# Optimization experiments

Hardware: AMD Instinct MI355X
Metric: run time of the kernel (lower is better)

The kernel has to match this reference:

```python
import jax, jax.numpy as jnp
import numpy as np

# Static configuration (matches init_kwargs)
L = 3264          # seq_length
K = 12            # ktc=4 -> K=12
LOCC = 4          # ktc=4 -> Locc=4
S, B, A = 8, 64, 4  # streams (user/port pairs), batch, rx antennas
DELAY_MIN, DELAY_MAX = -10, 10


def _phasor(m):
    # m: integer shifts [S, B] -> exp(1j*2*pi*m*n/L) as [S, B, L]
    n = jnp.arange(L, dtype=jnp.int32)
    ang = (2.0 * np.pi / L) * ((m[..., None] * n) % L).astype(jnp.float32)
    return jax.lax.complex(jnp.cos(ang), jnp.sin(ang))


def _linear_interp(h_avg):
    # np.interp with uniform source grid orig[i] = (LOCC-1)/2 + i*LOCC, clamped at ends.
    # h_avg: [S, B, A, R] complex, R = L // LOCC -> [S, B, A, L]
    R = L // LOCC
    new = jnp.arange(L, dtype=jnp.float32)
    t = jnp.clip((new - (LOCC - 1) / 2.0) / LOCC, 0.0, float(R - 1))
    i0 = jnp.floor(t).astype(jnp.int32)
    i1 = jnp.minimum(i0 + 1, R - 1)
    frac = (t - i0).astype(jnp.float32)
    return h_avg[..., i0] * (1.0 - frac) + h_avg[..., i1] * frac


def reference(ls_real, ls_imag, cyclic_shifts, noise_powers):
    ls = jax.lax.complex(ls_real, ls_imag)                     # [S,B,A,L]
    ideal_peak = ((K - cyclic_shifts) % K) * (L // K)          # [S]

    # Stage 1: IFFT + timing-offset search (torch.no_grad in original)
    h_time = jnp.fft.ifft(ls, axis=-1)
    power = jax.lax.stop_gradient(jnp.sum(jnp.abs(h_time) ** 2, axis=2))  # [S,B,L]
    offs = jnp.arange(DELAY_MIN, DELAY_MAX + 1, dtype=jnp.int32)          # [21]
    cand_idx = (ideal_peak[:, None] + offs[None, :]) % L                   # [S,21]
    cand_idx = jnp.broadcast_to(cand_idx[:, None, :], (S, B, offs.shape[0]))
    cand_pow = jnp.take_along_axis(power, cand_idx, axis=-1)               # [S,B,21]
    t_off = offs[jnp.argmax(cand_pow, axis=-1)]                            # [S,B]
    m = t_off + ideal_peak[:, None]                                        # [S,B]
    ph_m = _phasor(m)        # [S,B,L]
    ph_T = _phasor(t_off)    # [S,B,L]

    # Stage 2: phasor shift, OCC demux, interpolation (inside no_grad in original)
    h_shift = ls * ph_m[:, :, None, :]
    h_avg = h_shift.reshape(S, B, A, L // LOCC, LOCC).mean(-1)             # [S,B,A,L/4]
    h_interp = jax.lax.stop_gradient(_linear_interp(h_avg))                # [S,B,A,L]

    # Stage 3: global residual against stream (0,0)'s LS estimate
    total_recon = jnp.sum(h_interp * jnp.conj(ph_m)[:, :, None, :], axis=0)  # [B,A,L]
    residual = ls[0] - total_recon                                           # [B,A,L]

    # Stage 4: apply residual, MMSE (identity: mmse_module=None), timing recovery
    h_wr = h_interp + residual[None, :, :, None, :].squeeze(3) if False else h_interp + residual[None] * ph_m[:, :, None, :]
    final = h_wr * jnp.conj(ph_T)[:, :, None, :]                             # [S,B,A,L]
    return jnp.stack([final.real, final.imag]).astype(jnp.float32)          # [2,S,B,A,L]


def setup_inputs() -> dict:
    key = jax.random.key(0)
    k1, k2, k3, k4 = jax.random.split(key, 4)
    return {
        "ls_real": jax.random.normal(k1, (S, B, A, L), dtype=jnp.float32),
        "ls_imag": jax.random.normal(k2, (S, B, A, L), dtype=jnp.float32),
        "cyclic_shifts": jax.random.randint(k3, (S,), 0, K, dtype=jnp.int32),
        "noise_powers": jax.random.uniform(k4, (B,), dtype=jnp.float32),
    }
```

## Files before the change

kernel.cpp:

```cpp
#include <hip/hip_runtime.h>

namespace {

constexpr int L = 3264;
constexpr int K = 12;
constexpr int S = 8;
constexpr int B = 64;
constexpr int A = 4;
constexpr int R = 816;
constexpr int NOFF = 21;
constexpr int PEAK_STEP = L / K;
constexpr float TWO_PI = 6.28318530717958647692f;
constexpr float CINV = TWO_PI / (float)L;
constexpr int NCHUNK = (L + 255) / 256;

__device__ __forceinline__ float rfl(float x) {
    return __uint_as_float(__builtin_amdgcn_readfirstlane(__float_as_uint(x)));
}

__global__ __launch_bounds__(256)
void k_table(float2* __restrict__ tw)
{
    const int j = blockIdx.x * 256 + threadIdx.x;
    if (j < L) {
        float sv, cv;
        __sincosf(CINV * (float)j, &sv, &cv);
        tw[j] = make_float2(cv, sv);
    }
}

__global__ __launch_bounds__(256)
void k_dft(const float* __restrict__ lsr, const float* __restrict__ lsi,
           const int* __restrict__ cs, float* __restrict__ pow_out)
{
    __shared__ float2 red[4][NOFF];

    const int blk = blockIdx.x;
    const int sb = blk >> 2;
    const int a = blk & 3;
    const int s = sb >> 6;
    const int tid = threadIdx.x;
    const int lane = tid & 63;
    const int w = tid >> 6;

    const int ideal = ((K - cs[s]) % K) * PEAK_STEP;
    int idx0 = (ideal - 10) % L; if (idx0 < 0) idx0 += L;

    const int jb = (tid * idx0) % L;
    float br, bi; __sincosf(CINV * (float)jb, &bi, &br);
    float lr, li; __sincosf(CINV * (float)tid, &li, &lr);
    float pwr[NOFF], pwi[NOFF], ar[NOFF], ai[NOFF];
    pwr[0] = br; pwi[0] = bi;
    #pragma unroll
    for (int d = 1; d < NOFF; ++d) {
        pwr[d] = pwr[d-1] * lr - pwi[d-1] * li;
        pwi[d] = pwr[d-1] * li + pwi[d-1] * lr;
    }
    #pragma unroll
    for (int d = 0; d < NOFF; ++d) { ar[d] = 0.f; ai[d] = 0.f; }

    const int js = (256 * idx0) % L;
    float s0r, s0i; __sincosf(CINV * (float)js, &s0i, &s0r);
    float c8r, c8i; __sincosf(CINV * 256.0f, &c8i, &c8r);
    float str_[NOFF], sti_[NOFF];
    {
        float cr = s0r, ci = s0i;
        #pragma unroll
        for (int d = 0; d < NOFF; ++d) {
            str_[d] = rfl(cr); sti_[d] = rfl(ci);
            const float nr2 = cr * c8r - ci * c8i;
            ci = cr * c8i + ci * c8r;
            cr = nr2;
        }
    }

    const float* __restrict__ pr  = lsr + (size_t)blk * L;
    const float* __restrict__ pi_ = lsi + (size_t)blk * L;

    for (int it = 0; it < 12; ++it) {
        const float xr = pr[tid + (it << 8)];
        const float xi = pi_[tid + (it << 8)];
        #pragma unroll
        for (int d = 0; d < NOFF; ++d) {
            ar[d] += xr * pwr[d] - xi * pwi[d];
            ai[d] += xr * pwi[d] + xi * pwr[d];
            const float nr2 = pwr[d] * str_[d] - pwi[d] * sti_[d];
            pwi[d] = pwr[d] * sti_[d] + pwi[d] * str_[d];
            pwr[d] = nr2;
        }
    }
    if (tid < 192) {
        const float xr = pr[tid + 3072];
        const float xi = pi_[tid + 3072];
        #pragma unroll
        for (int d = 0; d < NOFF; ++d) {
            ar[d] += xr * pwr[d] - xi * pwi[d];
            ai[d] += xr * pwi[d] + xi * pwr[d];
        }
    }

    #pragma unroll
    for (int d = 0; d < NOFF; ++d) {
        float r = ar[d], im = ai[d];
        #pragma unroll
        for (int o = 32; o > 0; o >>= 1) {
            r  += __shfl_xor(r, o);
            im += __shfl_xor(im, o);
        }
        if (lane == 0) red[w][d] = make_float2(r, im);
    }
    __syncthreads();

    if (w == 0 && lane < NOFF) {
        float rr = 0.f, ii = 0.f;
        #pragma unroll
        for (int q = 0; q < 4; ++q) { rr += red[q][lane].x; ii += red[q][lane].y; }
        pow_out[sb * (NOFF * A) + lane * A + a] = rr * rr + ii * ii;
    }
}

__global__ __launch_bounds__(64)
void k_argmax(const float* __restrict__ pow_in, const int* __restrict__ cs,
              int* __restrict__ toff_out, int* __restrict__ m_out)
{
    const int sb = blockIdx.x;
    const int lane = threadIdx.x;
    const int s = sb >> 6;
    const int ideal = ((K - cs[s]) % K) * PEAK_STEP;

    float pw = -1.f;
    if (lane < NOFF) {
        const float4 p4 = *(const float4*)(pow_in + sb * (NOFF * A) + lane * A);
        pw = p4.x + p4.y + p4.z + p4.w;
    }
    float mx = pw;
    #pragma unroll
    for (int o = 32; o > 0; o >>= 1) mx = fmaxf(mx, __shfl_xor(mx, o));
    const unsigned long long msk = __ballot(pw == mx);
    const int argd = __ffsll(msk) - 1;
    if (lane == 0) {
        const int toff = argd - 10;
        toff_out[sb] = toff;
        m_out[sb]    = toff + ideal;
    }
}

__global__ __launch_bounds__(256)
void k_havg(const float* __restrict__ lsr, const float* __restrict__ lsi,
            const int* __restrict__ m_arr, const float2* __restrict__ tw,
            float2* __restrict__ havg)
{
    const int blk = blockIdx.x;
    const int sb = blk >> 2;
    const int tid = threadIdx.x;

    int mp = m_arr[sb] % L; if (mp < 0) mp += L;
    const float2 emp = tw[mp];

    const float4* __restrict__ qr4 = (const float4*)(lsr + (size_t)blk * L);
    const float4* __restrict__ qi4 = (const float4*)(lsi + (size_t)blk * L);
    float2* __restrict__ dst = havg + (size_t)blk * R;

    for (int i = tid; i < R; i += 256) {
        const int j = (mp * (4 * i)) % L;
        const float2 w0 = tw[j];
        const float4 xr = qr4[i];
        const float4 xi = qi4[i];
        float wr = w0.x, wi = w0.y;
        float are, aim, nr;
        are  = xr.x * wr - xi.x * wi;  aim  = xr.x * wi + xi.x * wr;
        nr = wr * emp.x - wi * emp.y;  wi = wr * emp.y + wi * emp.x;  wr = nr;
        are += xr.y * wr - xi.y * wi;  aim += xr.y * wi + xi.y * wr;
        nr = wr * emp.x - wi * emp.y;  wi = wr * emp.y + wi * emp.x;  wr = nr;
        are += xr.z * wr - xi.z * wi;  aim += xr.z * wi + xi.z * wr;
        nr = wr * emp.x - wi * emp.y;  wi = wr * emp.y + wi * emp.x;  wr = nr;
        are += xr.w * wr - xi.w * wi;  aim += xr.w * wi + xi.w * wr;
        dst[i] = make_float2(are * 0.25f, aim * 0.25f);
    }
}

__global__ __launch_bounds__(256)
void k_final(const float* __restrict__ lsr, const float* __restrict__ lsi,
             const int* __restrict__ toff_arr, const int* __restrict__ m_arr,
             const float2* __restrict__ havg, const float2* __restrict__ tw,
             float* __restrict__ out)
{
    __shared__ float2 twl[L];
    for (int j = threadIdx.x; j < L; j += 256) twl[j] = tw[j];
    __syncthreads();

    const int bid = blockIdx.x;
    const int chunk = bid % NCHUNK;
    const int ba = bid / NCHUNK;
    const int b = ba >> 2;
    const int a = ba & 3;
    const int l = chunk * 256 + (int)threadIdx.x;
    if (l >= L) return;

    float t = ((float)l - 1.5f) * 0.25f;
    t = fminf(fmaxf(t, 0.0f), (float)(R - 1));
    const int i0 = (int)t;
    const int i1 = min(i0 + 1, R - 1);
    const float frac = t - (float)i0;

    float hire[S], hiim[S], pmre[S], pmim[S];
    float rre = 0.f, rim = 0.f;

    #pragma unroll
    for (int s = 0; s < S; ++s) {
        const int sb = s * B + b;
        int mp = m_arr[sb] % L; if (mp < 0) mp += L;
        const float2 wm = twl[(mp * l) % L];
        const float2 h0 = havg[((size_t)sb * A + a) * R + i0];
        const float2 h1 = havg[((size_t)sb * A + a) * R + i1];
        const float hr = h0.x * (1.f - frac) + h1.x * frac;
        const float hi = h0.y * (1.f - frac) + h1.y * frac;
        hire[s] = hr; hiim[s] = hi; pmre[s] = wm.x; pmim[s] = wm.y;
        rre += hr * wm.x + hi * wm.y;
        rim += hi * wm.x - hr * wm.y;
    }

    const size_t off0 = ((size_t)(b * A + a)) * L + l;
    const float resre = lsr[off0] - rre;
    const float resim = lsi[off0] - rim;

    #pragma unroll
    for (int s = 0; s < S; ++s) {
        const float wre = hire[s] + resre * pmre[s] - resim * pmim[s];
        const float wim = hiim[s] + resre * pmim[s] + resim * pmre[s];
        int jt = (toff_arr[s * B + b] * l) % L; if (jt < 0) jt += L;
        const float2 wt = twl[jt];
        const float fre = wre * wt.x + wim * wt.y;
        const float fim = wim * wt.x - wre * wt.y;
        const size_t o = (((size_t)(s * B + b)) * A + a) * L + l;
        __builtin_nontemporal_store(fre, &out[o]);
        __builtin_nontemporal_store(fim, &out[(size_t)S * B * A * L + o]);
    }
}

}

extern "C" void kernel_launch(void* const* d_in, const int* in_sizes, int n_in,
                              void* d_out, int out_size, void* d_ws, size_t ws_size,
                              hipStream_t stream) {
    (void)in_sizes; (void)n_in; (void)out_size; (void)ws_size;
    const float* lsr = (const float*)d_in[0];
    const float* lsi = (const float*)d_in[1];
    const int*   cs  = (const int*)d_in[2];

    int* toff = (int*)d_ws;
    int* marr = toff + 512;
    float2* tw   = (float2*)((char*)d_ws + 4096);
    float*  powb = (float*)((char*)d_ws + 30720);
    float2* havg = (float2*)((char*)d_ws + 204800);

    k_table <<<NCHUNK, 256, 0, stream>>>(tw);
    k_dft   <<<S * B * A, 256, 0, stream>>>(lsr, lsi, cs, powb);
    k_argmax<<<S * B, 64, 0, stream>>>(powb, cs, toff, marr);
    k_havg  <<<S * B * A, 256, 0, stream>>>(lsr, lsi, marr, tw, havg);
    k_final <<<B * A * NCHUNK, 256, 0, stream>>>(lsr, lsi, toff, marr, havg, tw,
                                                 (float*)d_out);
}
```

Before: 168.6 us.

## Fuse OCC averaging into final kernel and split DFT bins across two blocks

Removes the separate h_avg kernel and its global round-trip. Each final block now computes the averaged channel values it needs for its chunk, with a one-sample halo, into shared memory. The DFT timing search now splits its 21 candidate bins into two blocks of 10 and 11, which doubles the block count and lowers register pressure, and it prefetches the next input sample to hide load latency. The cost is that every input row is read twice in the DFT stage, and the final kernel does extra loads and an extra barrier per block.

```diff
diff --git a/kernel.cpp b/kernel.cpp
--- a/kernel.cpp
+++ b/kernel.cpp
@@ -13,6 +13,7 @@
 constexpr float TWO_PI = 6.28318530717958647692f;
 constexpr float CINV = TWO_PI / (float)L;
 constexpr int NCHUNK = (L + 255) / 256;
+constexpr int HS_MAX = 66;
 
 __device__ __forceinline__ float rfl(float x) {
     return __uint_as_float(__builtin_amdgcn_readfirstlane(__float_as_uint(x)));
@@ -29,44 +30,32 @@
     }
 }
 
-__global__ __launch_bounds__(256)
-void k_dft(const float* __restrict__ lsr, const float* __restrict__ lsi,
-           const int* __restrict__ cs, float* __restrict__ pow_out)
-{
-    __shared__ float2 red[4][NOFF];
-
-    const int blk = blockIdx.x;
-    const int sb = blk >> 2;
-    const int a = blk & 3;
-    const int s = sb >> 6;
-    const int tid = threadIdx.x;
-    const int lane = tid & 63;
-    const int w = tid >> 6;
-
-    const int ideal = ((K - cs[s]) % K) * PEAK_STEP;
-    int idx0 = (ideal - 10) % L; if (idx0 < 0) idx0 += L;
-
-    const int jb = (tid * idx0) % L;
+template <int NB>
+__device__ __forceinline__ void dft_bins(
+    const float* __restrict__ pr, const float* __restrict__ pi_,
+    int idx0d0, int tid, int lane, int w, float2 (*red)[11])
+{
+    const int jb = (tid * idx0d0) % L;
     float br, bi; __sincosf(CINV * (float)jb, &bi, &br);
     float lr, li; __sincosf(CINV * (float)tid, &li, &lr);
-    float pwr[NOFF], pwi[NOFF], ar[NOFF], ai[NOFF];
+    float pwr[NB], pwi[NB], ar[NB], ai[NB];
     pwr[0] = br; pwi[0] = bi;
     #pragma unroll
-    for (int d = 1; d < NOFF; ++d) {
+    for (int d = 1; d < NB; ++d) {
         pwr[d] = pwr[d-1] * lr - pwi[d-1] * li;
         pwi[d] = pwr[d-1] * li + pwi[d-1] * lr;
     }
     #pragma unroll
-    for (int d = 0; d < NOFF; ++d) { ar[d] = 0.f; ai[d] = 0.f; }
-
-    const int js = (256 * idx0) % L;
+    for (int d = 0; d < NB; ++d) { ar[d] = 0.f; ai[d] = 0.f; }
+
+    const int js = (256 * idx0d0) % L;
     float s0r, s0i; __sincosf(CINV * (float)js, &s0i, &s0r);
     float c8r, c8i; __sincosf(CINV * 256.0f, &c8i, &c8r);
-    float str_[NOFF], sti_[NOFF];
+    float str_[NB], sti_[NB];
     {
         float cr = s0r, ci = s0i;
         #pragma unroll
-        for (int d = 0; d < NOFF; ++d) {
+        for (int d = 0; d < NB; ++d) {
             str_[d] = rfl(cr); sti_[d] = rfl(ci);
             const float nr2 = cr * c8r - ci * c8i;
             ci = cr * c8i + ci * c8r;
@@ -74,33 +63,36 @@
         }
     }
 
-    const float* __restrict__ pr  = lsr + (size_t)blk * L;
-    const float* __restrict__ pi_ = lsi + (size_t)blk * L;
-
+    float xr = pr[tid], xi = pi_[tid];
     for (int it = 0; it < 12; ++it) {
-        const float xr = pr[tid + (it << 8)];
-        const float xi = pi_[tid + (it << 8)];
-        #pragma unroll
-        for (int d = 0; d < NOFF; ++d) {
+        float nxr = 0.f, nxi = 0.f;
+        if (it < 11) {
+            nxr = pr[tid + ((it + 1) << 8)];
+            nxi = pi_[tid + ((it + 1) << 8)];
+        } else if (tid < 192) {
+            nxr = pr[tid + 3072];
+            nxi = pi_[tid + 3072];
+        }
+        #pragma unroll
+        for (int d = 0; d < NB; ++d) {
             ar[d] += xr * pwr[d] - xi * pwi[d];
             ai[d] += xr * pwi[d] + xi * pwr[d];
             const float nr2 = pwr[d] * str_[d] - pwi[d] * sti_[d];
             pwi[d] = pwr[d] * sti_[d] + pwi[d] * str_[d];
             pwr[d] = nr2;
         }
+        xr = nxr; xi = nxi;
     }
     if (tid < 192) {
-        const float xr = pr[tid + 3072];
-        const float xi = pi_[tid + 3072];
-        #pragma unroll
-        for (int d = 0; d < NOFF; ++d) {
+        #pragma unroll
+        for (int d = 0; d < NB; ++d) {
             ar[d] += xr * pwr[d] - xi * pwi[d];
             ai[d] += xr * pwi[d] + xi * pwr[d];
         }
     }
 
     #pragma unroll
-    for (int d = 0; d < NOFF; ++d) {
+    for (int d = 0; d < NB; ++d) {
         float r = ar[d], im = ai[d];
         #pragma unroll
         for (int o = 32; o > 0; o >>= 1) {
@@ -109,13 +101,42 @@
         }
         if (lane == 0) red[w][d] = make_float2(r, im);
     }
+}
+
+__global__ __launch_bounds__(256)
+void k_dft(const float* __restrict__ lsr, const float* __restrict__ lsi,
+           const int* __restrict__ cs, float* __restrict__ pow_out)
+{
+    __shared__ float2 red[4][11];
+
+    const int blk = blockIdx.x;
+    const int row = blk >> 1;
+    const int half = blk & 1;
+    const int sb = row >> 2;
+    const int a = row & 3;
+    const int s = sb >> 6;
+    const int tid = threadIdx.x;
+    const int lane = tid & 63;
+    const int w = tid >> 6;
+
+    const int ideal = ((K - cs[s]) % K) * PEAK_STEP;
+    int idx0 = (ideal - 10) % L; if (idx0 < 0) idx0 += L;
+    const int d0 = half ? 10 : 0;
+    const int idx0d0 = (idx0 + d0) % L;
+
+    const float* __restrict__ pr  = lsr + (size_t)row * L;
+    const float* __restrict__ pi_ = lsi + (size_t)row * L;
+
+    if (half) dft_bins<11>(pr, pi_, idx0d0, tid, lane, w, red);
+    else      dft_bins<10>(pr, pi_, idx0d0, tid, lane, w, red);
     __syncthreads();
 
-    if (w == 0 && lane < NOFF) {
+    const int NB = half ? 11 : 10;
+    if (w == 0 && lane < NB) {
         float rr = 0.f, ii = 0.f;
         #pragma unroll
         for (int q = 0; q < 4; ++q) { rr += red[q][lane].x; ii += red[q][lane].y; }
-        pow_out[sb * (NOFF * A) + lane * A + a] = rr * rr + ii * ii;
+        pow_out[sb * (NOFF * A) + (d0 + lane) * A + a] = rr * rr + ii * ii;
     }
 }
 
@@ -146,73 +167,76 @@
 }
 
 __global__ __launch_bounds__(256)
-void k_havg(const float* __restrict__ lsr, const float* __restrict__ lsi,
-            const int* __restrict__ m_arr, const float2* __restrict__ tw,
-            float2* __restrict__ havg)
-{
-    const int blk = blockIdx.x;
-    const int sb = blk >> 2;
-    const int tid = threadIdx.x;
-
-    int mp = m_arr[sb] % L; if (mp < 0) mp += L;
-    const float2 emp = tw[mp];
-
-    const float4* __restrict__ qr4 = (const float4*)(lsr + (size_t)blk * L);
-    const float4* __restrict__ qi4 = (const float4*)(lsi + (size_t)blk * L);
-    float2* __restrict__ dst = havg + (size_t)blk * R;
-
-    for (int i = tid; i < R; i += 256) {
-        const int j = (mp * (4 * i)) % L;
-        const float2 w0 = tw[j];
-        const float4 xr = qr4[i];
-        const float4 xi = qi4[i];
-        float wr = w0.x, wi = w0.y;
-        float are, aim, nr;
-        are  = xr.x * wr - xi.x * wi;  aim  = xr.x * wi + xi.x * wr;
-        nr = wr * emp.x - wi * emp.y;  wi = wr * emp.y + wi * emp.x;  wr = nr;
-        are += xr.y * wr - xi.y * wi;  aim += xr.y * wi + xi.y * wr;
-        nr = wr * emp.x - wi * emp.y;  wi = wr * emp.y + wi * emp.x;  wr = nr;
-        are += xr.z * wr - xi.z * wi;  aim += xr.z * wi + xi.z * wr;
-        nr = wr * emp.x - wi * emp.y;  wi = wr * emp.y + wi * emp.x;  wr = nr;
-        are += xr.w * wr - xi.w * wi;  aim += xr.w * wi + xi.w * wr;
-        dst[i] = make_float2(are * 0.25f, aim * 0.25f);
-    }
-}
-
-__global__ __launch_bounds__(256)
 void k_final(const float* __restrict__ lsr, const float* __restrict__ lsi,
              const int* __restrict__ toff_arr, const int* __restrict__ m_arr,
-             const float2* __restrict__ havg, const float2* __restrict__ tw,
-             float* __restrict__ out)
+             const float2* __restrict__ tw, float* __restrict__ out)
 {
     __shared__ float2 twl[L];
-    for (int j = threadIdx.x; j < L; j += 256) twl[j] = tw[j];
-    __syncthreads();
+    __shared__ float2 hs[S][HS_MAX];
+    __shared__ int mps[S], tfs[S];
 
     const int bid = blockIdx.x;
     const int chunk = bid % NCHUNK;
     const int ba = bid / NCHUNK;
     const int b = ba >> 2;
     const int a = ba & 3;
-    const int l = chunk * 256 + (int)threadIdx.x;
+    const int tid = threadIdx.x;
+
+    for (int j = tid; j < L; j += 256) twl[j] = tw[j];
+    if (tid < S) {
+        int mp = m_arr[tid * B + b] % L; if (mp < 0) mp += L;
+        mps[tid] = mp;
+        int tp = toff_arr[tid * B + b] % L; if (tp < 0) tp += L;
+        tfs[tid] = tp;
+    }
+    __syncthreads();
+
+    const int imin = max(0, chunk * 64 - 1);
+    const int imax = min(R - 1, chunk * 64 + 64);
+    const int cnt = imax - imin + 1;
+
+    for (int t = tid; t < S * HS_MAX; t += 256) {
+        const int s = t / HS_MAX;
+        const int ii = t % HS_MAX;
+        if (ii < cnt) {
+            const int i = imin + ii;
+            const int sb = s * B + b;
+            const int mp = mps[s];
+            const float2 emp = twl[mp];
+            const float2 w0 = twl[(mp * (4 * i)) % L];
+            const float4 xr = *(const float4*)(lsr + ((size_t)sb * A + a) * L + 4 * i);
+            const float4 xi = *(const float4*)(lsi + ((size_t)sb * A + a) * L + 4 * i);
+            float wr = w0.x, wi = w0.y;
+            float are, aim, nr;
+            are  = xr.x * wr - xi.x * wi;  aim  = xr.x * wi + xi.x * wr;
+            nr = wr * emp.x - wi * emp.y;  wi = wr * emp.y + wi * emp.x;  wr = nr;
+            are += xr.y * wr - xi.y * wi;  aim += xr.y * wi + xi.y * wr;
+            nr = wr * emp.x - wi * emp.y;  wi = wr * emp.y + wi * emp.x;  wr = nr;
+            are += xr.z * wr - xi.z * wi;  aim += xr.z * wi + xi.z * wr;
+            nr = wr * emp.x - wi * emp.y;  wi = wr * emp.y + wi * emp.x;  wr = nr;
+            are += xr.w * wr - xi.w * wi;  aim += xr.w * wi + xi.w * wr;
+            hs[s][ii] = make_float2(are * 0.25f, aim * 0.25f);
+        }
+    }
+    __syncthreads();
+
+    const int l = chunk * 256 + tid;
     if (l >= L) return;
 
-    float t = ((float)l - 1.5f) * 0.25f;
-    t = fminf(fmaxf(t, 0.0f), (float)(R - 1));
-    const int i0 = (int)t;
+    float t2 = ((float)l - 1.5f) * 0.25f;
+    t2 = fminf(fmaxf(t2, 0.0f), (float)(R - 1));
+    const int i0 = (int)t2;
     const int i1 = min(i0 + 1, R - 1);
-    const float frac = t - (float)i0;
+    const float frac = t2 - (float)i0;
 
     float hire[S], hiim[S], pmre[S], pmim[S];
     float rre = 0.f, rim = 0.f;
 
     #pragma unroll
     for (int s = 0; s < S; ++s) {
-        const int sb = s * B + b;
-        int mp = m_arr[sb] % L; if (mp < 0) mp += L;
-        const float2 wm = twl[(mp * l) % L];
-        const float2 h0 = havg[((size_t)sb * A + a) * R + i0];
-        const float2 h1 = havg[((size_t)sb * A + a) * R + i1];
+        const float2 wm = twl[(mps[s] * l) % L];
+        const float2 h0 = hs[s][i0 - imin];
+        const float2 h1 = hs[s][i1 - imin];
         const float hr = h0.x * (1.f - frac) + h1.x * frac;
         const float hi = h0.y * (1.f - frac) + h1.y * frac;
         hire[s] = hr; hiim[s] = hi; pmre[s] = wm.x; pmim[s] = wm.y;
@@ -228,8 +252,7 @@
     for (int s = 0; s < S; ++s) {
         const float wre = hire[s] + resre * pmre[s] - resim * pmim[s];
         const float wim = hiim[s] + resre * pmim[s] + resim * pmre[s];
-        int jt = (toff_arr[s * B + b] * l) % L; if (jt < 0) jt += L;
-        const float2 wt = twl[jt];
+        const float2 wt = twl[(tfs[s] * l) % L];
         const float fre = wre * wt.x + wim * wt.y;
         const float fim = wim * wt.x - wre * wt.y;
         const size_t o = (((size_t)(s * B + b)) * A + a) * L + l;
@@ -252,12 +275,10 @@
     int* marr = toff + 512;
     float2* tw   = (float2*)((char*)d_ws + 4096);
     float*  powb = (float*)((char*)d_ws + 30720);
-    float2* havg = (float2*)((char*)d_ws + 204800);
 
     k_table <<<NCHUNK, 256, 0, stream>>>(tw);
-    k_dft   <<<S * B * A, 256, 0, stream>>>(lsr, lsi, cs, powb);
+    k_dft   <<<S * B * A * 2, 256, 0, stream>>>(lsr, lsi, cs, powb);
     k_argmax<<<S * B, 64, 0, stream>>>(powb, cs, toff, marr);
-    k_havg  <<<S * B * A, 256, 0, stream>>>(lsr, lsi, marr, tw, havg);
-    k_final <<<B * A * NCHUNK, 256, 0, stream>>>(lsr, lsi, toff, marr, havg, tw,
+    k_final <<<B * A * NCHUNK, 256, 0, stream>>>(lsr, lsi, toff, marr, tw,
                                                  (float*)d_out);
 }
```

Measured after the change: 178.6 us. +5.9%, slower.
